# Kernel optimization log

Hardware: AMD Instinct MI355X
Metric: run time of the kernel (lower is better)

## Reference

```python
import jax, jax.numpy as jnp
import numpy as np

B, N, C, H, D, K = 8, 2000, 64, 64, 16, 2  # batch, nodes, hidden, hidden_hidden, embed_dim, cheb_k


def setup_inputs() -> dict:
    key = jax.random.key(0)
    ks = jax.random.split(key, 12)
    f = lambda k, s, sc=1.0: jax.random.normal(k, s, dtype=jnp.float32) * sc
    return {
        "z": f(ks[0], (B, N, C)),
        "W_in": f(ks[1], (H, C), 0.1),
        "b_in": f(ks[2], (H,), 0.1),
        "W_out": f(ks[3], (C * C, H), 0.05),
        "b_out": f(ks[4], (C * C,), 0.05),
        "emb": f(ks[5], (N, D), 0.1),
        "wp": f(ks[6], (D, K, H, H), 0.1),
        "bp": f(ks[7], (D, H), 0.1),
        "w1": f(ks[8], (C,)),
        "w2": f(ks[9], (C,)),
        "vs": f(ks[10], (N, N), 0.02),
        "bs": f(ks[11], (N, N), 0.02),
    }


def reference(z, W_in, b_in, W_out, b_out, emb, wp, bp, w1, w2, vs, bs):
    # linear_in + relu: (B,N,C) -> (B,N,H)
    h = jax.nn.relu(jnp.einsum("bnc,hc->bnh", z, W_in) + b_in)

    # data-adaptive graph: softmax over rows of relu(emb @ emb^T)
    A = jax.nn.softmax(jax.nn.relu(emb @ emb.T), axis=1)  # (N,N)
    S = jnp.stack([jnp.eye(N, dtype=z.dtype), A], axis=0)  # (K,N,N), cheb_k=2

    # spatial attention on h (x = h.unsqueeze(1), f_in == H == C)
    e1 = h @ w1  # (B,N)
    e2 = h @ w2  # (B,N)
    prod = e1[:, :, None] * e2[:, None, :]  # (B,N,N) outer product
    E = jax.nn.softmax(
        jnp.einsum("nm,bmp->bnp", vs, jax.nn.sigmoid(prod + bs)), axis=-1
    )  # (B,N,N)

    # batched supports: E.unsqueeze(1) @ S -> (B,K,N,N)
    sup = jnp.einsum("bnm,kmp->bknp", E, S)

    # node-adaptive weights / bias
    weights = jnp.einsum("nd,dkio->nkio", emb, wp)  # (N,K,H,H)
    bias = emb @ bp  # (N,H)

    # graph conv
    x_g = jnp.einsum("bknm,bmc->bnkc", sup, h)  # (B,N,K,H)
    g = jnp.einsum("bnki,nkio->bno", x_g, weights) + bias  # (B,N,H)

    # linear_out + view + tanh, scaled by 0.1
    out = jnp.tanh(jnp.einsum("bnh,oh->bno", g, W_out) + b_out)
    return 0.1 * out.reshape(B, N, C, C)
```

## Files before the change

### kernel.cpp

```cpp
#include <hip/hip_runtime.h>
#include <hip/hip_bf16.h>

#define NN 2000
#define NP 2048
#define BB 8
#define HH 64
#define DD 16

typedef __hip_bfloat16 bf16;
typedef short bf16x8 __attribute__((ext_vector_type(8)));
typedef float f32x4 __attribute__((ext_vector_type(4)));

__device__ __forceinline__ float fast_sigmoid(float x) {
    return 1.0f / (1.0f + __expf(-x));
}
__device__ __forceinline__ float fast_tanh(float x) {
    float e = __expf(2.0f * x);
    return 1.0f - 2.0f / (e + 1.0f);
}

__device__ __forceinline__ void glds16(const void* g, void* l) {
    __builtin_amdgcn_global_load_lds(
        (const __attribute__((address_space(1))) void*)g,
        (__attribute__((address_space(3))) void*)l, 16, 0, 0);
}

__global__ __launch_bounds__(256) void k_h(
        const float* __restrict__ z, const float* __restrict__ W_in,
        const float* __restrict__ b_in, const float* __restrict__ w1,
        const float* __restrict__ w2, float* __restrict__ h,
        float* __restrict__ e1, float* __restrict__ e2) {
    __shared__ float WT[64 * 65];
    __shared__ float zs[4][64];
    int t = threadIdx.x;
    int lane = t & 63, ty = t >> 6;
    int bn0 = blockIdx.x * 4;
    for (int i = t; i < 64 * 64; i += 256) {
        int hh = i >> 6, c = i & 63;
        WT[c * 65 + hh] = W_in[i];
    }
    zs[ty][lane] = z[(size_t)(bn0 + ty) * 64 + lane];
    __syncthreads();
    float acc = b_in[lane];
    #pragma unroll
    for (int c = 0; c < 64; c++) acc += zs[ty][c] * WT[c * 65 + lane];
    float hv = fmaxf(acc, 0.0f);
    h[(size_t)(bn0 + ty) * 64 + lane] = hv;
    float p1 = hv * w1[lane], p2 = hv * w2[lane];
    #pragma unroll
    for (int off = 32; off > 0; off >>= 1) {
        p1 += __shfl_down(p1, off);
        p2 += __shfl_down(p2, off);
    }
    if (lane == 0) { e1[bn0 + ty] = p1; e2[bn0 + ty] = p2; }
}

__global__ __launch_bounds__(256) void k_A(const float* __restrict__ emb,
                                           bf16* __restrict__ A) {
    int i = blockIdx.x, t = threadIdx.x;
    if (i >= NN) {
        for (int j = t; j < NP; j += 256) A[(size_t)i * NP + j] = __float2bfloat16(0.0f);
        return;
    }
    __shared__ float ei[DD];
    __shared__ float rowbuf[NP];
    __shared__ float red[256];
    if (t < DD) ei[t] = emb[i * DD + t];
    __syncthreads();
    float lmax = -1e30f;
    for (int j = t; j < NP; j += 256) {
        float s = 0.0f;
        if (j < NN) {
            #pragma unroll
            for (int d = 0; d < DD; d++) s += ei[d] * emb[j * DD + d];
            s = fmaxf(s, 0.0f);
            lmax = fmaxf(lmax, s);
        }
        rowbuf[j] = s;
    }
    red[t] = lmax; __syncthreads();
    for (int o = 128; o > 0; o >>= 1) { if (t < o) red[t] = fmaxf(red[t], red[t + o]); __syncthreads(); }
    float mx = red[0];
    __syncthreads();
    float lsum = 0.0f;
    for (int j = t; j < NN; j += 256) {
        float e = __expf(rowbuf[j] - mx);
        rowbuf[j] = e; lsum += e;
    }
    red[t] = lsum; __syncthreads();
    for (int o = 128; o > 0; o >>= 1) { if (t < o) red[t] += red[t + o]; __syncthreads(); }
    float inv = 1.0f / red[0];
    for (int j = t; j < NP; j += 256)
        A[(size_t)i * NP + j] = __float2bfloat16(j < NN ? rowbuf[j] * inv : 0.0f);
}

__global__ void k_cvt_vs(const float* __restrict__ vs, bf16* __restrict__ out) {
    int id = blockIdx.x * 256 + threadIdx.x;
    int n = id >> 11, m = id & (NP - 1);
    float v = (n < NN && m < NN) ? vs[n * NN + m] : 0.0f;
    out[id] = __float2bfloat16(v);
}

__global__ void k_cvt_wout(const float* __restrict__ W_out, bf16* __restrict__ out) {
    int id = blockIdx.x * 256 + threadIdx.x;
    out[id] = __float2bfloat16(W_out[id]);
}

__global__ __launch_bounds__(256) void k_wn(const float* __restrict__ emb,
                                            const float* __restrict__ wp,
                                            float* __restrict__ Wn_all) {
    __shared__ float embs[128 * 16];
    int t = threadIdx.x;
    int n0 = blockIdx.x * 128;
    int jo = blockIdx.y * 256 + t;
    float wv[16];
    #pragma unroll
    for (int d = 0; d < 16; d++) wv[d] = wp[(size_t)d * 8192 + jo];
    for (int s = t; s < 128 * 16; s += 256) {
        int i = s >> 4, d = s & 15;
        int n = n0 + i;
        embs[s] = (n < NN) ? emb[n * 16 + d] : 0.f;
    }
    __syncthreads();
    for (int i = 0; i < 128; i++) {
        int n = n0 + i;
        if (n >= NN) break;
        const f32x4* ev = (const f32x4*)&embs[i * 16];
        f32x4 e0 = ev[0], e1 = ev[1], e2 = ev[2], e3 = ev[3];
        float a = 0.f;
        #pragma unroll
        for (int q = 0; q < 4; q++) a += e0[q] * wv[q];
        #pragma unroll
        for (int q = 0; q < 4; q++) a += e1[q] * wv[4 + q];
        #pragma unroll
        for (int q = 0; q < 4; q++) a += e2[q] * wv[8 + q];
        #pragma unroll
        for (int q = 0; q < 4; q++) a += e3[q] * wv[12 + q];
        Wn_all[(size_t)n * 8192 + jo] = a;
    }
}

__global__ __launch_bounds__(256) void k_hT(const float* __restrict__ h,
                                            bf16* __restrict__ hTcat,
                                            bf16* __restrict__ hsT) {
    __shared__ float tile[64 * 65];
    int nt = blockIdx.x, b = blockIdx.y;
    int tx = threadIdx.x & 63, ty = threadIdx.x >> 6;
    int n0 = nt * 64;
    for (int i = ty * 16; i < ty * 16 + 16; i++) {
        int n = n0 + i;
        tile[i * 65 + tx] = (n < NN) ? h[((size_t)b * NN + n) * 64 + tx] : 0.0f;
    }
    __syncthreads();
    for (int i = ty * 16; i < ty * 16 + 16; i++) {
        bf16 v = __float2bfloat16(tile[tx * 65 + i]);
        hTcat[((size_t)b * 64 + i) * NP + n0 + tx] = v;
        hsT[((size_t)b * 128 + i) * NP + n0 + tx] = v;
    }
}

__global__ __launch_bounds__(256) void k_AhT(const float* __restrict__ Ahcat,
                                             bf16* __restrict__ hsT) {
    __shared__ float tile[64 * 65];
    int pt = blockIdx.x, b = blockIdx.y;
    int tx = threadIdx.x & 63, ty = threadIdx.x >> 6;
    int p0 = pt * 64, q0 = b * 64;
    for (int i = ty * 16; i < ty * 16 + 16; i++)
        tile[i * 65 + tx] = Ahcat[((size_t)p0 + i) * 512 + q0 + tx];
    __syncthreads();
    for (int i = ty * 16; i < ty * 16 + 16; i++)
        hsT[((size_t)b * 128 + 64 + i) * NP + p0 + tx] =
            __float2bfloat16(tile[tx * 65 + i]);
}

__global__ __launch_bounds__(256) void k_Tt(const float* __restrict__ e1,
                                            const float* __restrict__ e2,
                                            const float* __restrict__ bs,
                                            bf16* __restrict__ Tt) {
    __shared__ float tile[64 * 65];
    int b = blockIdx.z;
    e1 += (size_t)b * NN;
    e2 += (size_t)b * NN;
    Tt += (size_t)b * NP * NP;
    int mt = blockIdx.x, pt = blockIdx.y;
    int tx = threadIdx.x & 63, ty = threadIdx.x >> 6;
    int m0 = mt * 64, p0 = pt * 64;
    int p = p0 + tx;
    float e2v = (p < NN) ? e2[p] : 0.0f;
    for (int i = ty * 16; i < ty * 16 + 16; i++) {
        int m = m0 + i;
        float v = 0.0f;
        if (m < NN && p < NN)
            v = fast_sigmoid(e1[m] * e2v + bs[(size_t)m * NN + p]);
        tile[i * 65 + tx] = v;
    }
    __syncthreads();
    for (int i = ty * 16; i < ty * 16 + 16; i++)
        Tt[((size_t)p0 + i) * NP + m0 + tx] = __float2bfloat16(tile[tx * 65 + i]);
}

__global__ __launch_bounds__(512) void k_gemm256pv(
        const bf16* __restrict__ X, const bf16* __restrict__ Yt,
        const bf16* __restrict__ hsT, float* __restrict__ xgPart,
        float* __restrict__ rsPart,
        int K, int ldx, int ldy, long long sY, long long sHs) {
    __shared__ short LDSb[65536];
    short* Asb = LDSb;
    short* Bsb = LDSb + 32768;
    int z = blockIdx.z;
    const bf16* Xp = X;
    const bf16* Yp = Yt + (long long)z * sY;
    int tid = threadIdx.x;
    int m0 = blockIdx.x * 256, n0 = blockIdx.y * 256;
    int wave = tid >> 6, lane = tid & 63;
    int wr = wave >> 2, wc = wave & 3;
    int fr = lane & 15, kq = lane >> 4;

    f32x4 zero = {0.f, 0.f, 0.f, 0.f};
    f32x4 acc[8][4];
    #pragma unroll
    for (int i = 0; i < 8; i++)
        #pragma unroll
        for (int j = 0; j < 4; j++) acc[i][j] = zero;

    int r8 = tid >> 3;
    int sslot = (tid & 7) ^ (r8 & 7);
    const bf16* xsrc = Xp + (long long)(m0 + r8) * ldx + sslot * 8;
    const bf16* ysrc = Yp + (long long)(n0 + r8) * ldy + sslot * 8;

    auto STAGE = [&](int tile) {
        short* Ab = Asb + (tile & 1) * 16384 + tid * 8;
        short* Bb = Bsb + (tile & 1) * 16384 + tid * 8;
        int ko = tile * 64;
        #pragma unroll
        for (int c = 0; c < 4; c++) {
            glds16(xsrc + (long long)(c * 64) * ldx + ko, Ab + c * 4096);
            glds16(ysrc + (long long)(c * 64) * ldy + ko, Bb + c * 4096);
        }
    };

    int NT = K >> 6;
    STAGE(0);
    STAGE(1);
    asm volatile("s_waitcnt vmcnt(8)" ::: "memory");
    __builtin_amdgcn_s_barrier();

    for (int t = 0; t < NT; t++) {
        const short* Ab = Asb + (t & 1) * 16384 + wr * 8192 + fr * 64;
        const short* Bb = Bsb + (t & 1) * 16384 + wc * 4096 + fr * 64;
        #pragma unroll
        for (int ks = 0; ks < 2; ks++) {
            int s = ((ks * 4 + kq) ^ (fr & 7)) * 8;
            bf16x8 a[8], b[4];
            #pragma unroll
            for (int i = 0; i < 8; i++)
                a[i] = *(const bf16x8*)(Ab + i * 1024 + s);
            #pragma unroll
            for (int j = 0; j < 4; j++)
                b[j] = *(const bf16x8*)(Bb + j * 1024 + s);
            __builtin_amdgcn_s_setprio(1);
            #pragma unroll
            for (int i = 0; i < 8; i++)
                #pragma unroll
                for (int j = 0; j < 4; j++)
                    acc[i][j] = __builtin_amdgcn_mfma_f32_16x16x32_bf16(a[i], b[j], acc[i][j], 0, 0, 0);
            __builtin_amdgcn_s_setprio(0);
        }
        __builtin_amdgcn_sched_barrier(0);
        __builtin_amdgcn_s_barrier();
        __builtin_amdgcn_sched_barrier(0);
        if (t + 2 < NT) {
            STAGE(t + 2);
            asm volatile("s_waitcnt vmcnt(8)" ::: "memory");
            __builtin_amdgcn_s_barrier();
        } else if (t + 1 < NT) {
            asm volatile("s_waitcnt vmcnt(0)" ::: "memory");
            __builtin_amdgcn_s_barrier();
        }
    }

    int rq = kq * 4;
    #pragma unroll
    for (int i = 0; i < 8; i++) {
        #pragma unroll
        for (int r = 0; r < 4; r++) {
            int lrow = wr * 128 + i * 16 + rq + r;
            float rs = 0.f;
            #pragma unroll
            for (int j = 0; j < 4; j++) {
                int lcol = wc * 64 + j * 16 + fr;
                float e = (n0 + lcol < NN) ? __expf(acc[i][j][r]) : 0.f;
                bf16 bv = __float2bfloat16(e);
                int sl = (lcol >> 3) ^ (lrow & 7);
                LDSb[lrow * 256 + sl * 8 + (lcol & 7)] = *(short*)&bv;
                rs += e;
            }
            rs += __shfl_xor(rs, 1);
            rs += __shfl_xor(rs, 2);
            rs += __shfl_xor(rs, 4);
            rs += __shfl_xor(rs, 8);
            if (fr == 0)
                rsPart[((long long)z * 32 + blockIdx.y * 4 + wc) * NP + m0 + lrow] = rs;
        }
    }
    __syncthreads();

    const bf16* hz = hsT + (long long)z * sHs;
    int wr2 = wave >> 2, wc2 = wave & 3;
    f32x4 acc2[8][2];
    #pragma unroll
    for (int i = 0; i < 8; i++)
        #pragma unroll
        for (int jj = 0; jj < 2; jj++) acc2[i][jj] = zero;
    #pragma unroll
    for (int ks = 0; ks < 8; ks++) {
        bf16x8 a2[8], b2[2];
        #pragma unroll
        for (int i = 0; i < 8; i++) {
            int row = wr2 * 128 + i * 16 + fr;
            int sl = (ks * 4 + kq) ^ (row & 7);
            a2[i] = *(const bf16x8*)(LDSb + row * 256 + sl * 8);
        }
        #pragma unroll
        for (int jj = 0; jj < 2; jj++)
            b2[jj] = *(const bf16x8*)(hz + (long long)(wc2 * 32 + jj * 16 + fr) * NP
                                      + n0 + ks * 32 + kq * 8);
        #pragma unroll
        for (int i = 0; i < 8; i++)
            #pragma unroll
            for (int jj = 0; jj < 2; jj++)
                acc2[i][jj] = __builtin_amdgcn_mfma_f32_16x16x32_bf16(a2[i], b2[jj], acc2[i][jj], 0, 0, 0);
    }
    long long slab = (long long)blockIdx.y * ((long long)BB * NP * 128);
    #pragma unroll
    for (int i = 0; i < 8; i++)
        #pragma unroll
        for (int jj = 0; jj < 2; jj++) {
            int jcol = wc2 * 32 + jj * 16 + fr;
            #pragma unroll
            for (int r = 0; r < 4; r++) {
                int n = m0 + wr2 * 128 + i * 16 + rq + r;
                xgPart[slab + ((long long)z * NP + n) * 128 + jcol] = acc2[i][jj][r];
            }
        }
}

template<bool TANH, int KSPLIT>
__global__ __launch_bounds__(256) void k_gemm_bt(
        const bf16* __restrict__ X, const bf16* __restrict__ Yt,
        float* __restrict__ C, const float* __restrict__ bias,
        int K, int ldx, int ldy, int ldc,
        long long sX, long long sY, long long sC, long long sSlice) {
    __shared__ short As[128 * 32];
    __shared__ short Bs[128 * 32];
    int zz = blockIdx.z;
    int ks = 0;
    if (KSPLIT > 1) { ks = zz % KSPLIT; zz /= KSPLIT; }
    const bf16* Xp = X + (long long)zz * sX;
    const bf16* Yp = Yt + (long long)zz * sY;
    float* Cp = C + (long long)zz * sC + (long long)ks * sSlice;
    int tid = threadIdx.x;
    int m0 = blockIdx.x * 128, n0 = blockIdx.y * 128;
    int wave = tid >> 6, lane = tid & 63;
    int wm = (wave >> 1) * 64, wn = (wave & 1) * 64;
    int fr = lane & 15, kq = lane >> 4;

    f32x4 zero = {0.f, 0.f, 0.f, 0.f};
    f32x4 acc[4][4];
    #pragma unroll
    for (int i = 0; i < 4; i++)
        #pragma unroll
        for (int j = 0; j < 4; j++) acc[i][j] = zero;

    int lrow = lane >> 2, lcol = (lane & 3) * 8;
    const bf16* xg0 = Xp + (long long)(m0 + wave * 16 + lrow) * ldx + lcol;
    const bf16* xg1 = xg0 + (long long)64 * ldx;
    const bf16* yg0 = Yp + (long long)(n0 + wave * 16 + lrow) * ldy + lcol;
    const bf16* yg1 = yg0 + (long long)64 * ldy;
    short* lA0 = As + wave * 512;
    short* lA1 = As + (wave + 4) * 512;
    short* lB0 = Bs + wave * 512;
    short* lB1 = Bs + (wave + 4) * 512;

    int kbeg = (KSPLIT > 1) ? ks * (K / KSPLIT) : 0;
    int kend = kbeg + K / KSPLIT;
    for (int k0 = kbeg; k0 < kend; k0 += 32) {
        __syncthreads();
        glds16(xg0 + k0, lA0);
        glds16(xg1 + k0, lA1);
        glds16(yg0 + k0, lB0);
        glds16(yg1 + k0, lB1);
        __syncthreads();
        bf16x8 a[4], b[4];
        #pragma unroll
        for (int i = 0; i < 4; i++)
            a[i] = *(const bf16x8*)(As + (wm + i * 16 + fr) * 32 + kq * 8);
        #pragma unroll
        for (int j = 0; j < 4; j++)
            b[j] = *(const bf16x8*)(Bs + (wn + j * 16 + fr) * 32 + kq * 8);
        #pragma unroll
        for (int i = 0; i < 4; i++)
            #pragma unroll
            for (int j = 0; j < 4; j++)
                acc[i][j] = __builtin_amdgcn_mfma_f32_16x16x32_bf16(a[i], b[j], acc[i][j], 0, 0, 0);
    }
    int rq = kq * 4;
    for (int i = 0; i < 4; i++)
        for (int j = 0; j < 4; j++) {
            int col = n0 + wn + j * 16 + fr;
            float bv = TANH ? bias[col] : 0.0f;
            #pragma unroll
            for (int r = 0; r < 4; r++) {
                int row = m0 + wm + i * 16 + rq + r;
                float v = acc[i][j][r];
                Cp[(long long)row * ldc + col] =
                    TANH ? 0.1f * fast_tanh(v + bv) : v;
            }
        }
}

__global__ __launch_bounds__(256) void k_reduce4(const float* __restrict__ part,
                                                 float* __restrict__ out, int total) {
    int i = (blockIdx.x * 256 + threadIdx.x) * 4;
    f32x4 a = *(const f32x4*)(part + i);
    f32x4 b = *(const f32x4*)(part + (size_t)total + i);
    f32x4 c = *(const f32x4*)(part + (size_t)2 * total + i);
    f32x4 d = *(const f32x4*)(part + (size_t)3 * total + i);
    *(f32x4*)(out + i) = (a + b) + (c + d);
}

__global__ __launch_bounds__(256) void k_reduce8(const float* __restrict__ part,
                                                 float* __restrict__ out, int total) {
    int i = (blockIdx.x * 256 + threadIdx.x) * 4;
    f32x4 s = *(const f32x4*)(part + i);
    #pragma unroll
    for (int k = 1; k < 8; k++)
        s += *(const f32x4*)(part + (size_t)k * total + i);
    *(f32x4*)(out + i) = s;
}

__global__ __launch_bounds__(256) void k_g(
        const float* __restrict__ Wn_all, const float* __restrict__ bp,
        const float* __restrict__ emb, const float* __restrict__ xg,
        const float* __restrict__ rsPart, bf16* __restrict__ gbf) {
    __shared__ float Wn[8192];
    __shared__ float xgs[1024];
    __shared__ float biass[64];
    __shared__ float invs[8];
    int n = blockIdx.x, t = threadIdx.x;
    if (t < 8) {
        float s = 0.f;
        #pragma unroll
        for (int y = 0; y < 32; y++)
            s += rsPart[((size_t)t * 32 + y) * NP + n];
        invs[t] = 1.0f / s;
    }
    if (t >= 64 && t < 128) {
        int o = t - 64;
        float a = 0.f;
        #pragma unroll
        for (int d = 0; d < 16; d++) a += emb[n * 16 + d] * bp[d * 64 + o];
        biass[o] = a;
    }
    {
        const f32x4* src = (const f32x4*)(Wn_all + (size_t)n * 8192);
        f32x4* dst = (f32x4*)Wn;
        #pragma unroll
        for (int s = 0; s < 8; s++) dst[s * 256 + t] = src[s * 256 + t];
    }
    __syncthreads();
    for (int s = 0; s < 4; s++) {
        int id = t + s * 256;
        int b = id >> 7, j = id & 127;
        xgs[id] = xg[((size_t)b * NP + n) * 128 + j] * invs[b];
    }
    __syncthreads();
    int o = t & 63, bh = t >> 6;
    for (int half = 0; half < 2; half++) {
        int b = bh + half * 4;
        float a = biass[o];
        for (int j = 0; j < 128; j++) a += xgs[b * 128 + j] * Wn[j * 64 + o];
        gbf[((size_t)b * NN + n) * 64 + o] = __float2bfloat16(a);
    }
}

extern "C" void kernel_launch(void* const* d_in, const int* in_sizes, int n_in,
                              void* d_out, int out_size, void* d_ws, size_t ws_size,
                              hipStream_t stream) {
    const float* z     = (const float*)d_in[0];
    const float* W_in  = (const float*)d_in[1];
    const float* b_in  = (const float*)d_in[2];
    const float* W_out = (const float*)d_in[3];
    const float* b_out = (const float*)d_in[4];
    const float* emb   = (const float*)d_in[5];
    const float* wp    = (const float*)d_in[6];
    const float* bp    = (const float*)d_in[7];
    const float* w1    = (const float*)d_in[8];
    const float* w2    = (const float*)d_in[9];
    const float* vs    = (const float*)d_in[10];
    const float* bs    = (const float*)d_in[11];

    char* p = (char*)d_ws;
    auto alloc = [&](size_t bytes) -> char* {
        char* r = p;
        p += (bytes + 255) & ~(size_t)255;
        return r;
    };
    float* h       = (float*)alloc((size_t)BB * NN * 64 * 4);
    float* e1      = (float*)alloc((size_t)BB * NN * 4);
    float* e2      = (float*)alloc((size_t)BB * NN * 4);
    bf16*  A_bf    = (bf16*) alloc((size_t)NP * NP * 2);
    bf16*  vs_bf   = (bf16*) alloc((size_t)NP * NP * 2);
    bf16*  Tt_all  = (bf16*) alloc((size_t)BB * NP * NP * 2);
    float* rsPart  = (float*)alloc((size_t)BB * 32 * NP * 4);
    bf16*  hTcat   = (bf16*) alloc((size_t)512 * NP * 2);
    float* Ahcat   = (float*)alloc((size_t)NP * 512 * 4);
    float* AhPart  = (float*)alloc((size_t)4 * NP * 512 * 4);
    bf16*  hsT     = (bf16*) alloc((size_t)BB * 128 * NP * 2);
    float* xg      = (float*)alloc((size_t)BB * NP * 128 * 4);
    float* xgPart8 = (float*)alloc((size_t)8 * BB * NP * 128 * 4);
    bf16*  gbf     = (bf16*) alloc((size_t)BB * NN * 64 * 2);
    bf16*  Wo_bf   = (bf16*) alloc((size_t)4096 * 64 * 2);
    float* Wn_all  = (float*)alloc((size_t)NN * 8192 * 4);

    k_h<<<BB * NN / 4, 256, 0, stream>>>(z, W_in, b_in, w1, w2, h, e1, e2);
    k_A<<<NP, 256, 0, stream>>>(emb, A_bf);
    k_cvt_vs<<<(NP * NP) / 256, 256, 0, stream>>>(vs, vs_bf);
    k_cvt_wout<<<(4096 * 64) / 256, 256, 0, stream>>>(W_out, Wo_bf);
    k_wn<<<dim3(16, 32), 256, 0, stream>>>(emb, wp, Wn_all);
    k_hT<<<dim3(NP / 64, BB), 256, 0, stream>>>(h, hTcat, hsT);

    k_gemm_bt<false, 4><<<dim3(16, 4, 4), 256, 0, stream>>>(
        A_bf, hTcat, AhPart, nullptr, NP, NP, NP, 512,
        0, 0, 0, (long long)NP * 512);
    k_reduce4<<<(NP * 512) / 1024, 256, 0, stream>>>(AhPart, Ahcat, NP * 512);
    k_AhT<<<dim3(NP / 64, BB), 256, 0, stream>>>(Ahcat, hsT);

    k_Tt<<<dim3(NP / 64, NP / 64, BB), 256, 0, stream>>>(e1, e2, bs, Tt_all);
    k_gemm256pv<<<dim3(8, 8, BB), 512, 0, stream>>>(
        vs_bf, Tt_all, hsT, xgPart8, rsPart, NP, NP, NP,
        (long long)NP * NP, (long long)128 * NP);
    k_reduce8<<<(BB * NP * 128) / 1024, 256, 0, stream>>>(xgPart8, xg, BB * NP * 128);

    k_g<<<NN, 256, 0, stream>>>(Wn_all, bp, emb, xg, rsPart, gbf);
    k_gemm_bt<true, 1><<<dim3(125, 32, 1), 256, 0, stream>>>(
        gbf, Wo_bf, (float*)d_out, b_out, 64, 64, 64, 4096, 0, 0, 0, 0);
}
```

Before: 646.5 us.

## Restructure big GEMM pipeline, merge prep kernels, fold reduction into graph conv

Three preprocessing kernels are merged into one launch via block-index dispatch. The main 256x256 GEMM is reworked to stage half-K (32-wide) slices with a new swizzle, interleaving the prefetch of the next tile's A/B halves between MFMA groups separated by barriers. The separate k_reduce8 over xgPart is removed by having k_g sum the eight partials directly, and the A@h GEMM split-K goes from 4 to 8. The aim is fewer launches, less extra memory traffic and better load/compute overlap, at the cost of more barriers per tile and larger partial buffers.

Result: no change. 650.8 us (+0.7%).

```diff
diff --git a/kernel.cpp b/kernel.cpp
--- a/kernel.cpp
+++ b/kernel.cpp
@@ -94,25 +94,28 @@
         A[(size_t)i * NP + j] = __float2bfloat16(j < NN ? rowbuf[j] * inv : 0.0f);
 }
 
-__global__ void k_cvt_vs(const float* __restrict__ vs, bf16* __restrict__ out) {
-    int id = blockIdx.x * 256 + threadIdx.x;
-    int n = id >> 11, m = id & (NP - 1);
-    float v = (n < NN && m < NN) ? vs[n * NN + m] : 0.0f;
-    out[id] = __float2bfloat16(v);
-}
-
-__global__ void k_cvt_wout(const float* __restrict__ W_out, bf16* __restrict__ out) {
-    int id = blockIdx.x * 256 + threadIdx.x;
-    out[id] = __float2bfloat16(W_out[id]);
-}
-
-__global__ __launch_bounds__(256) void k_wn(const float* __restrict__ emb,
-                                            const float* __restrict__ wp,
-                                            float* __restrict__ Wn_all) {
+__global__ __launch_bounds__(256) void k_misc(
+        const float* __restrict__ vs, bf16* __restrict__ vs_bf,
+        const float* __restrict__ W_out, bf16* __restrict__ Wo_bf,
+        const float* __restrict__ emb, const float* __restrict__ wp,
+        float* __restrict__ Wn_all) {
     __shared__ float embs[128 * 16];
-    int t = threadIdx.x;
-    int n0 = blockIdx.x * 128;
-    int jo = blockIdx.y * 256 + t;
+    int bid = blockIdx.x, t = threadIdx.x;
+    if (bid < 16384) {
+        int id = bid * 256 + t;
+        int n = id >> 11, m = id & (NP - 1);
+        float v = (n < NN && m < NN) ? vs[n * NN + m] : 0.0f;
+        vs_bf[id] = __float2bfloat16(v);
+        return;
+    }
+    if (bid < 16384 + 1024) {
+        int id = (bid - 16384) * 256 + t;
+        Wo_bf[id] = __float2bfloat16(W_out[id]);
+        return;
+    }
+    int wb = bid - 17408;
+    int n0 = (wb & 15) * 128;
+    int jo = (wb >> 4) * 256 + t;
     float wv[16];
     #pragma unroll
     for (int d = 0; d < 16; d++) wv[d] = wp[(size_t)d * 8192 + jo];
@@ -205,6 +208,7 @@
         float* __restrict__ rsPart,
         int K, int ldx, int ldy, long long sY, long long sHs) {
     __shared__ short LDSb[65536];
+    __shared__ float rsum2[4][256];
     short* Asb = LDSb;
     short* Bsb = LDSb + 32768;
     int z = blockIdx.z;
@@ -223,61 +227,113 @@
         #pragma unroll
         for (int j = 0; j < 4; j++) acc[i][j] = zero;
 
-    int r8 = tid >> 3;
-    int sslot = (tid & 7) ^ (r8 & 7);
-    const bf16* xsrc = Xp + (long long)(m0 + r8) * ldx + sslot * 8;
-    const bf16* ysrc = Yp + (long long)(n0 + r8) * ldy + sslot * 8;
-
-    auto STAGE = [&](int tile) {
-        short* Ab = Asb + (tile & 1) * 16384 + tid * 8;
-        short* Bb = Bsb + (tile & 1) * 16384 + tid * 8;
-        int ko = tile * 64;
-        #pragma unroll
-        for (int c = 0; c < 4; c++) {
-            glds16(xsrc + (long long)(c * 64) * ldx + ko, Ab + c * 4096);
-            glds16(ysrc + (long long)(c * 64) * ldy + ko, Bb + c * 4096);
-        }
+    int r4 = tid >> 2, slot = tid & 3;
+    int scol = (slot ^ ((r4 >> 1) & 3)) * 8;
+    const bf16* xsrc = Xp + (long long)(m0 + r4) * ldx + scol;
+    const bf16* ysrc = Yp + (long long)(n0 + r4) * ldy + scol;
+    short* Ad = Asb + tid * 8;
+    short* Bd = Bsb + tid * 8;
+
+    auto SA = [&](int tile, int kh) {
+        short* d = Ad + (tile & 1) * 16384 + kh * 8192;
+        long long ko = tile * 64 + kh * 32;
+        glds16(xsrc + ko, d);
+        glds16(xsrc + 128 * (long long)ldx + ko, d + 4096);
     };
+    auto SB = [&](int tile, int kh) {
+        short* d = Bd + (tile & 1) * 16384 + kh * 8192;
+        long long ko = tile * 64 + kh * 32;
+        glds16(ysrc + ko, d);
+        glds16(ysrc + 128 * (long long)ldy + ko, d + 4096);
+    };
+
+    int aoff[8], boff[4];
+    #pragma unroll
+    for (int i = 0; i < 8; i++) {
+        int row = wr * 128 + i * 16 + fr;
+        aoff[i] = row * 32 + ((kq ^ ((row >> 1) & 3)) << 3);
+    }
+    #pragma unroll
+    for (int j = 0; j < 4; j++) {
+        int row = wc * 64 + j * 16 + fr;
+        boff[j] = row * 32 + ((kq ^ ((row >> 1) & 3)) << 3);
+    }
 
     int NT = K >> 6;
-    STAGE(0);
-    STAGE(1);
-    asm volatile("s_waitcnt vmcnt(8)" ::: "memory");
+    SA(0, 0); SB(0, 0); SA(0, 1); SB(0, 1);
+    asm volatile("s_waitcnt vmcnt(4)" ::: "memory");
     __builtin_amdgcn_s_barrier();
 
     for (int t = 0; t < NT; t++) {
-        const short* Ab = Asb + (t & 1) * 16384 + wr * 8192 + fr * 64;
-        const short* Bb = Bsb + (t & 1) * 16384 + wc * 4096 + fr * 64;
-        #pragma unroll
-        for (int ks = 0; ks < 2; ks++) {
-            int s = ((ks * 4 + kq) ^ (fr & 7)) * 8;
-            bf16x8 a[8], b[4];
-            #pragma unroll
-            for (int i = 0; i < 8; i++)
-                a[i] = *(const bf16x8*)(Ab + i * 1024 + s);
-            #pragma unroll
-            for (int j = 0; j < 4; j++)
-                b[j] = *(const bf16x8*)(Bb + j * 1024 + s);
-            __builtin_amdgcn_s_setprio(1);
-            #pragma unroll
-            for (int i = 0; i < 8; i++)
-                #pragma unroll
-                for (int j = 0; j < 4; j++)
-                    acc[i][j] = __builtin_amdgcn_mfma_f32_16x16x32_bf16(a[i], b[j], acc[i][j], 0, 0, 0);
-            __builtin_amdgcn_s_setprio(0);
-        }
-        __builtin_amdgcn_sched_barrier(0);
-        __builtin_amdgcn_s_barrier();
-        __builtin_amdgcn_sched_barrier(0);
-        if (t + 2 < NT) {
-            STAGE(t + 2);
-            asm volatile("s_waitcnt vmcnt(8)" ::: "memory");
-            __builtin_amdgcn_s_barrier();
-        } else if (t + 1 < NT) {
-            asm volatile("s_waitcnt vmcnt(0)" ::: "memory");
-            __builtin_amdgcn_s_barrier();
-        }
-    }
+        int bs0 = (t & 1) * 16384;
+        int bs1 = bs0 + 8192;
+        bool pf = (t + 1 < NT);
+        bf16x8 a[8], b[4];
+        #pragma unroll
+        for (int i = 0; i < 8; i++) a[i] = *(const bf16x8*)(Asb + bs0 + aoff[i]);
+        b[0] = *(const bf16x8*)(Bsb + bs0 + boff[0]);
+        b[1] = *(const bf16x8*)(Bsb + bs0 + boff[1]);
+        if (pf) SA(t + 1, 0);
+        __builtin_amdgcn_s_barrier();
+        __builtin_amdgcn_sched_barrier(0);
+        __builtin_amdgcn_s_setprio(1);
+        #pragma unroll
+        for (int i = 0; i < 8; i++) {
+            acc[i][0] = __builtin_amdgcn_mfma_f32_16x16x32_bf16(a[i], b[0], acc[i][0], 0, 0, 0);
+            acc[i][1] = __builtin_amdgcn_mfma_f32_16x16x32_bf16(a[i], b[1], acc[i][1], 0, 0, 0);
+        }
+        __builtin_amdgcn_s_setprio(0);
+        __builtin_amdgcn_sched_barrier(0);
+        __builtin_amdgcn_s_barrier();
+        b[2] = *(const bf16x8*)(Bsb + bs0 + boff[2]);
+        b[3] = *(const bf16x8*)(Bsb + bs0 + boff[3]);
+        if (pf) SB(t + 1, 0);
+        __builtin_amdgcn_s_barrier();
+        __builtin_amdgcn_sched_barrier(0);
+        __builtin_amdgcn_s_setprio(1);
+        #pragma unroll
+        for (int i = 0; i < 8; i++) {
+            acc[i][2] = __builtin_amdgcn_mfma_f32_16x16x32_bf16(a[i], b[2], acc[i][2], 0, 0, 0);
+            acc[i][3] = __builtin_amdgcn_mfma_f32_16x16x32_bf16(a[i], b[3], acc[i][3], 0, 0, 0);
+        }
+        __builtin_amdgcn_s_setprio(0);
+        __builtin_amdgcn_sched_barrier(0);
+        if (pf) asm volatile("s_waitcnt vmcnt(4)" ::: "memory");
+        else    asm volatile("s_waitcnt vmcnt(0)" ::: "memory");
+        __builtin_amdgcn_s_barrier();
+        #pragma unroll
+        for (int i = 0; i < 8; i++) a[i] = *(const bf16x8*)(Asb + bs1 + aoff[i]);
+        b[0] = *(const bf16x8*)(Bsb + bs1 + boff[0]);
+        b[1] = *(const bf16x8*)(Bsb + bs1 + boff[1]);
+        if (pf) SA(t + 1, 1);
+        __builtin_amdgcn_s_barrier();
+        __builtin_amdgcn_sched_barrier(0);
+        __builtin_amdgcn_s_setprio(1);
+        #pragma unroll
+        for (int i = 0; i < 8; i++) {
+            acc[i][0] = __builtin_amdgcn_mfma_f32_16x16x32_bf16(a[i], b[0], acc[i][0], 0, 0, 0);
+            acc[i][1] = __builtin_amdgcn_mfma_f32_16x16x32_bf16(a[i], b[1], acc[i][1], 0, 0, 0);
+        }
+        __builtin_amdgcn_s_setprio(0);
+        __builtin_amdgcn_sched_barrier(0);
+        __builtin_amdgcn_s_barrier();
+        b[2] = *(const bf16x8*)(Bsb + bs1 + boff[2]);
+        b[3] = *(const bf16x8*)(Bsb + bs1 + boff[3]);
+        if (pf) SB(t + 1, 1);
+        __builtin_amdgcn_s_barrier();
+        __builtin_amdgcn_sched_barrier(0);
+        __builtin_amdgcn_s_setprio(1);
+        #pragma unroll
+        for (int i = 0; i < 8; i++) {
+            acc[i][2] = __builtin_amdgcn_mfma_f32_16x16x32_bf16(a[i], b[2], acc[i][2], 0, 0, 0);
+            acc[i][3] = __builtin_amdgcn_mfma_f32_16x16x32_bf16(a[i], b[3], acc[i][3], 0, 0, 0);
+        }
+        __builtin_amdgcn_s_setprio(0);
+        __builtin_amdgcn_sched_barrier(0);
+        if (pf) asm volatile("s_waitcnt vmcnt(4)" ::: "memory");
+        __builtin_amdgcn_s_barrier();
+    }
+    __syncthreads();
 
     int rq = kq * 4;
     #pragma unroll
@@ -419,16 +475,6 @@
         }
 }
 
-__global__ __launch_bounds__(256) void k_reduce4(const float* __restrict__ part,
-                                                 float* __restrict__ out, int total) {
-    int i = (blockIdx.x * 256 + threadIdx.x) * 4;
-    f32x4 a = *(const f32x4*)(part + i);
-    f32x4 b = *(const f32x4*)(part + (size_t)total + i);
-    f32x4 c = *(const f32x4*)(part + (size_t)2 * total + i);
-    f32x4 d = *(const f32x4*)(part + (size_t)3 * total + i);
-    *(f32x4*)(out + i) = (a + b) + (c + d);
-}
-
 __global__ __launch_bounds__(256) void k_reduce8(const float* __restrict__ part,
                                                  float* __restrict__ out, int total) {
     int i = (blockIdx.x * 256 + threadIdx.x) * 4;
@@ -441,12 +487,13 @@
 
 __global__ __launch_bounds__(256) void k_g(
         const float* __restrict__ Wn_all, const float* __restrict__ bp,
-        const float* __restrict__ emb, const float* __restrict__ xg,
+        const float* __restrict__ emb, const float* __restrict__ xgPart,
         const float* __restrict__ rsPart, bf16* __restrict__ gbf) {
     __shared__ float Wn[8192];
     __shared__ float xgs[1024];
     __shared__ float biass[64];
     __shared__ float invs[8];
+    const long long TOT = (long long)BB * NP * 128;
     int n = blockIdx.x, t = threadIdx.x;
     if (t < 8) {
         float s = 0.f;
@@ -472,7 +519,11 @@
     for (int s = 0; s < 4; s++) {
         int id = t + s * 256;
         int b = id >> 7, j = id & 127;
-        xgs[id] = xg[((size_t)b * NP + n) * 128 + j] * invs[b];
+        long long base = ((long long)b * NP + n) * 128 + j;
+        float a = 0.f;
+        #pragma unroll
+        for (int sl = 0; sl < 8; sl++) a += xgPart[sl * TOT + base];
+        xgs[id] = a * invs[b];
     }
     __syncthreads();
     int o = t & 63, bh = t >> 6;
@@ -515,9 +566,8 @@
     float* rsPart  = (float*)alloc((size_t)BB * 32 * NP * 4);
     bf16*  hTcat   = (bf16*) alloc((size_t)512 * NP * 2);
     float* Ahcat   = (float*)alloc((size_t)NP * 512 * 4);
-    float* AhPart  = (float*)alloc((size_t)4 * NP * 512 * 4);
+    float* AhPart  = (float*)alloc((size_t)8 * NP * 512 * 4);
     bf16*  hsT     = (bf16*) alloc((size_t)BB * 128 * NP * 2);
-    float* xg      = (float*)alloc((size_t)BB * NP * 128 * 4);
     float* xgPart8 = (float*)alloc((size_t)8 * BB * NP * 128 * 4);
     bf16*  gbf     = (bf16*) alloc((size_t)BB * NN * 64 * 2);
     bf16*  Wo_bf   = (bf16*) alloc((size_t)4096 * 64 * 2);
@@ -525,24 +575,22 @@
 
     k_h<<<BB * NN / 4, 256, 0, stream>>>(z, W_in, b_in, w1, w2, h, e1, e2);
     k_A<<<NP, 256, 0, stream>>>(emb, A_bf);
-    k_cvt_vs<<<(NP * NP) / 256, 256, 0, stream>>>(vs, vs_bf);
-    k_cvt_wout<<<(4096 * 64) / 256, 256, 0, stream>>>(W_out, Wo_bf);
-    k_wn<<<dim3(16, 32), 256, 0, stream>>>(emb, wp, Wn_all);
+    k_misc<<<16384 + 1024 + 512, 256, 0, stream>>>(vs, vs_bf, W_out, Wo_bf,
+                                                   emb, wp, Wn_all);
     k_hT<<<dim3(NP / 64, BB), 256, 0, stream>>>(h, hTcat, hsT);
 
-    k_gemm_bt<false, 4><<<dim3(16, 4, 4), 256, 0, stream>>>(
+    k_gemm_bt<false, 8><<<dim3(16, 4, 8), 256, 0, stream>>>(
         A_bf, hTcat, AhPart, nullptr, NP, NP, NP, 512,
         0, 0, 0, (long long)NP * 512);
-    k_reduce4<<<(NP * 512) / 1024, 256, 0, stream>>>(AhPart, Ahcat, NP * 512);
+    k_reduce8<<<(NP * 512) / 1024, 256, 0, stream>>>(AhPart, Ahcat, NP * 512);
     k_AhT<<<dim3(NP / 64, BB), 256, 0, stream>>>(Ahcat, hsT);
 
     k_Tt<<<dim3(NP / 64, NP / 64, BB), 256, 0, stream>>>(e1, e2, bs, Tt_all);
     k_gemm256pv<<<dim3(8, 8, BB), 512, 0, stream>>>(
         vs_bf, Tt_all, hsT, xgPart8, rsPart, NP, NP, NP,
         (long long)NP * NP, (long long)128 * NP);
-    k_reduce8<<<(BB * NP * 128) / 1024, 256, 0, stream>>>(xgPart8, xg, BB * NP * 128);
-
-    k_g<<<NN, 256, 0, stream>>>(Wn_all, bp, emb, xg, rsPart, gbf);
+
+    k_g<<<NN, 256, 0, stream>>>(Wn_all, bp, emb, xgPart8, rsPart, gbf);
     k_gemm_bt<true, 1><<<dim3(125, 32, 1), 256, 0, stream>>>(
         gbf, Wo_bf, (float*)d_out, b_out, 64, 64, 64, 4096, 0, 0, 0, 0);
 }
```

## Merge prep kernels, reuse bs tile across batch, remap GEMM blocks per XCD

Applied to the files above, without the earlier changes.

Folds the vs/W_out conversions and the node-weight kernel into one launch. k_Tt now reads each bs tile once and loops over the batch instead of re-reading bs per batch. The main fused GEMM uses a 1-D grid remapped so blocks sharing operands land on the same XCD. The xg split-K reduction moves into k_g, and the A·h GEMM split-K goes from 4 to 8. Together these cut launch count and HBM traffic, at the cost of more partial-buffer traffic and less parallelism in k_Tt.

After: 655.5 us. Within noise of the previous version (+1.4%).

```diff
diff --git a/kernel.cpp b/kernel.cpp
--- a/kernel.cpp
+++ b/kernel.cpp
@@ -94,25 +94,28 @@
         A[(size_t)i * NP + j] = __float2bfloat16(j < NN ? rowbuf[j] * inv : 0.0f);
 }
 
-__global__ void k_cvt_vs(const float* __restrict__ vs, bf16* __restrict__ out) {
-    int id = blockIdx.x * 256 + threadIdx.x;
-    int n = id >> 11, m = id & (NP - 1);
-    float v = (n < NN && m < NN) ? vs[n * NN + m] : 0.0f;
-    out[id] = __float2bfloat16(v);
-}
-
-__global__ void k_cvt_wout(const float* __restrict__ W_out, bf16* __restrict__ out) {
-    int id = blockIdx.x * 256 + threadIdx.x;
-    out[id] = __float2bfloat16(W_out[id]);
-}
-
-__global__ __launch_bounds__(256) void k_wn(const float* __restrict__ emb,
-                                            const float* __restrict__ wp,
-                                            float* __restrict__ Wn_all) {
+__global__ __launch_bounds__(256) void k_misc(
+        const float* __restrict__ vs, bf16* __restrict__ vs_bf,
+        const float* __restrict__ W_out, bf16* __restrict__ Wo_bf,
+        const float* __restrict__ emb, const float* __restrict__ wp,
+        float* __restrict__ Wn_all) {
     __shared__ float embs[128 * 16];
-    int t = threadIdx.x;
-    int n0 = blockIdx.x * 128;
-    int jo = blockIdx.y * 256 + t;
+    int bid = blockIdx.x, t = threadIdx.x;
+    if (bid < 16384) {
+        int id = bid * 256 + t;
+        int n = id >> 11, m = id & (NP - 1);
+        float v = (n < NN && m < NN) ? vs[n * NN + m] : 0.0f;
+        vs_bf[id] = __float2bfloat16(v);
+        return;
+    }
+    if (bid < 16384 + 1024) {
+        int id = (bid - 16384) * 256 + t;
+        Wo_bf[id] = __float2bfloat16(W_out[id]);
+        return;
+    }
+    int wb = bid - 17408;
+    int n0 = (wb & 15) * 128;
+    int jo = (wb >> 4) * 256 + t;
     float wv[16];
     #pragma unroll
     for (int d = 0; d < 16; d++) wv[d] = wp[(size_t)d * 8192 + jo];
@@ -177,26 +180,32 @@
                                             const float* __restrict__ e2,
                                             const float* __restrict__ bs,
                                             bf16* __restrict__ Tt) {
+    __shared__ float bst[64 * 65];
     __shared__ float tile[64 * 65];
-    int b = blockIdx.z;
-    e1 += (size_t)b * NN;
-    e2 += (size_t)b * NN;
-    Tt += (size_t)b * NP * NP;
     int mt = blockIdx.x, pt = blockIdx.y;
     int tx = threadIdx.x & 63, ty = threadIdx.x >> 6;
     int m0 = mt * 64, p0 = pt * 64;
     int p = p0 + tx;
-    float e2v = (p < NN) ? e2[p] : 0.0f;
     for (int i = ty * 16; i < ty * 16 + 16; i++) {
         int m = m0 + i;
-        float v = 0.0f;
-        if (m < NN && p < NN)
-            v = fast_sigmoid(e1[m] * e2v + bs[(size_t)m * NN + p]);
-        tile[i * 65 + tx] = v;
-    }
-    __syncthreads();
-    for (int i = ty * 16; i < ty * 16 + 16; i++)
-        Tt[((size_t)p0 + i) * NP + m0 + tx] = __float2bfloat16(tile[tx * 65 + i]);
+        bst[i * 65 + tx] = (m < NN && p < NN) ? bs[(size_t)m * NN + p] : 0.0f;
+    }
+    __syncthreads();
+    for (int b = 0; b < BB; b++) {
+        float e2v = (p < NN) ? e2[b * NN + p] : 0.0f;
+        for (int i = ty * 16; i < ty * 16 + 16; i++) {
+            int m = m0 + i;
+            float v = 0.0f;
+            if (m < NN && p < NN)
+                v = fast_sigmoid(e1[b * NN + m] * e2v + bst[i * 65 + tx]);
+            tile[i * 65 + tx] = v;
+        }
+        __syncthreads();
+        for (int i = ty * 16; i < ty * 16 + 16; i++)
+            Tt[(size_t)b * NP * NP + ((size_t)p0 + i) * NP + m0 + tx] =
+                __float2bfloat16(tile[tx * 65 + i]);
+        __syncthreads();
+    }
 }
 
 __global__ __launch_bounds__(512) void k_gemm256pv(
@@ -207,11 +216,16 @@
     __shared__ short LDSb[65536];
     short* Asb = LDSb;
     short* Bsb = LDSb + 32768;
-    int z = blockIdx.z;
+    int id = blockIdx.x;
+    int xcd = id & 7, jj0 = id >> 3;
+    int member = jj0 & 7, glocal = jj0 >> 3;
+    int group = glocal * 8 + xcd;
+    int bx = member, by = group & 7, bz = group >> 3;
+    int z = bz;
     const bf16* Xp = X;
     const bf16* Yp = Yt + (long long)z * sY;
     int tid = threadIdx.x;
-    int m0 = blockIdx.x * 256, n0 = blockIdx.y * 256;
+    int m0 = bx * 256, n0 = by * 256;
     int wave = tid >> 6, lane = tid & 63;
     int wr = wave >> 2, wc = wave & 3;
     int fr = lane & 15, kq = lane >> 4;
@@ -278,6 +292,7 @@
             __builtin_amdgcn_s_barrier();
         }
     }
+    __syncthreads();
 
     int rq = kq * 4;
     #pragma unroll
@@ -300,7 +315,7 @@
             rs += __shfl_xor(rs, 4);
             rs += __shfl_xor(rs, 8);
             if (fr == 0)
-                rsPart[((long long)z * 32 + blockIdx.y * 4 + wc) * NP + m0 + lrow] = rs;
+                rsPart[((long long)z * 32 + by * 4 + wc) * NP + m0 + lrow] = rs;
         }
     }
     __syncthreads();
@@ -331,7 +346,7 @@
             for (int jj = 0; jj < 2; jj++)
                 acc2[i][jj] = __builtin_amdgcn_mfma_f32_16x16x32_bf16(a2[i], b2[jj], acc2[i][jj], 0, 0, 0);
     }
-    long long slab = (long long)blockIdx.y * ((long long)BB * NP * 128);
+    long long slab = (long long)by * ((long long)BB * NP * 128);
     #pragma unroll
     for (int i = 0; i < 8; i++)
         #pragma unroll
@@ -419,16 +434,6 @@
         }
 }
 
-__global__ __launch_bounds__(256) void k_reduce4(const float* __restrict__ part,
-                                                 float* __restrict__ out, int total) {
-    int i = (blockIdx.x * 256 + threadIdx.x) * 4;
-    f32x4 a = *(const f32x4*)(part + i);
-    f32x4 b = *(const f32x4*)(part + (size_t)total + i);
-    f32x4 c = *(const f32x4*)(part + (size_t)2 * total + i);
-    f32x4 d = *(const f32x4*)(part + (size_t)3 * total + i);
-    *(f32x4*)(out + i) = (a + b) + (c + d);
-}
-
 __global__ __launch_bounds__(256) void k_reduce8(const float* __restrict__ part,
                                                  float* __restrict__ out, int total) {
     int i = (blockIdx.x * 256 + threadIdx.x) * 4;
@@ -441,12 +446,13 @@
 
 __global__ __launch_bounds__(256) void k_g(
         const float* __restrict__ Wn_all, const float* __restrict__ bp,
-        const float* __restrict__ emb, const float* __restrict__ xg,
+        const float* __restrict__ emb, const float* __restrict__ xgPart,
         const float* __restrict__ rsPart, bf16* __restrict__ gbf) {
     __shared__ float Wn[8192];
     __shared__ float xgs[1024];
     __shared__ float biass[64];
     __shared__ float invs[8];
+    const long long TOT = (long long)BB * NP * 128;
     int n = blockIdx.x, t = threadIdx.x;
     if (t < 8) {
         float s = 0.f;
@@ -472,7 +478,11 @@
     for (int s = 0; s < 4; s++) {
         int id = t + s * 256;
         int b = id >> 7, j = id & 127;
-        xgs[id] = xg[((size_t)b * NP + n) * 128 + j] * invs[b];
+        long long base = ((long long)b * NP + n) * 128 + j;
+        float a = 0.f;
+        #pragma unroll
+        for (int sl = 0; sl < 8; sl++) a += xgPart[sl * TOT + base];
+        xgs[id] = a * invs[b];
     }
     __syncthreads();
     int o = t & 63, bh = t >> 6;
@@ -515,9 +525,8 @@
     float* rsPart  = (float*)alloc((size_t)BB * 32 * NP * 4);
     bf16*  hTcat   = (bf16*) alloc((size_t)512 * NP * 2);
     float* Ahcat   = (float*)alloc((size_t)NP * 512 * 4);
-    float* AhPart  = (float*)alloc((size_t)4 * NP * 512 * 4);
+    float* AhPart  = (float*)alloc((size_t)8 * NP * 512 * 4);
     bf16*  hsT     = (bf16*) alloc((size_t)BB * 128 * NP * 2);
-    float* xg      = (float*)alloc((size_t)BB * NP * 128 * 4);
     float* xgPart8 = (float*)alloc((size_t)8 * BB * NP * 128 * 4);
     bf16*  gbf     = (bf16*) alloc((size_t)BB * NN * 64 * 2);
     bf16*  Wo_bf   = (bf16*) alloc((size_t)4096 * 64 * 2);
@@ -525,24 +534,22 @@
 
     k_h<<<BB * NN / 4, 256, 0, stream>>>(z, W_in, b_in, w1, w2, h, e1, e2);
     k_A<<<NP, 256, 0, stream>>>(emb, A_bf);
-    k_cvt_vs<<<(NP * NP) / 256, 256, 0, stream>>>(vs, vs_bf);
-    k_cvt_wout<<<(4096 * 64) / 256, 256, 0, stream>>>(W_out, Wo_bf);
-    k_wn<<<dim3(16, 32), 256, 0, stream>>>(emb, wp, Wn_all);
+    k_misc<<<16384 + 1024 + 512, 256, 0, stream>>>(vs, vs_bf, W_out, Wo_bf,
+                                                   emb, wp, Wn_all);
     k_hT<<<dim3(NP / 64, BB), 256, 0, stream>>>(h, hTcat, hsT);
 
-    k_gemm_bt<false, 4><<<dim3(16, 4, 4), 256, 0, stream>>>(
+    k_gemm_bt<false, 8><<<dim3(16, 4, 8), 256, 0, stream>>>(
         A_bf, hTcat, AhPart, nullptr, NP, NP, NP, 512,
         0, 0, 0, (long long)NP * 512);
-    k_reduce4<<<(NP * 512) / 1024, 256, 0, stream>>>(AhPart, Ahcat, NP * 512);
+    k_reduce8<<<(NP * 512) / 1024, 256, 0, stream>>>(AhPart, Ahcat, NP * 512);
     k_AhT<<<dim3(NP / 64, BB), 256, 0, stream>>>(Ahcat, hsT);
 
-    k_Tt<<<dim3(NP / 64, NP / 64, BB), 256, 0, stream>>>(e1, e2, bs, Tt_all);
-    k_gemm256pv<<<dim3(8, 8, BB), 512, 0, stream>>>(
+    k_Tt<<<dim3(NP / 64, NP / 64), 256, 0, stream>>>(e1, e2, bs, Tt_all);
+    k_gemm256pv<<<512, 512, 0, stream>>>(
         vs_bf, Tt_all, hsT, xgPart8, rsPart, NP, NP, NP,
         (long long)NP * NP, (long long)128 * NP);
-    k_reduce8<<<(BB * NP * 128) / 1024, 256, 0, stream>>>(xgPart8, xg, BB * NP * 128);
-
-    k_g<<<NN, 256, 0, stream>>>(Wn_all, bp, emb, xg, rsPart, gbf);
+
+    k_g<<<NN, 256, 0, stream>>>(Wn_all, bp, emb, xgPart8, rsPart, gbf);
     k_gemm_bt<true, 1><<<dim3(125, 32, 1), 256, 0, stream>>>(
         gbf, Wo_bf, (float*)d_out, b_out, 64, 64, 64, 4096, 0, 0, 0, 0);
 }
```
